# Kernel optimization log

Measured on AMD Instinct MI355X. Metric: run time of the kernel, lower is better.

Reference implementation:

```python
import jax, jax.numpy as jnp
import numpy as np
from jax import lax

SCALE = 1.0
DENSE = 4
ITERS = 5


def setup_inputs() -> dict:
    key = jax.random.key(0)
    k1, k2, k3 = jax.random.split(key, 3)
    N, C, H, W = 32, 3, 512, 512
    A = 512
    data = jax.random.normal(k1, (N, C, H, W), dtype=jnp.float32)
    attx = jax.random.uniform(k2, (N, A), dtype=jnp.float32)
    atty = jax.random.uniform(k3, (N, A), dtype=jnp.float32)
    return {"data": data, "attx": attx, "atty": atty}


def _water_fill(attx, atty, out_size, out_sizey, in_size):
    # iterative water-filling clamp: 5 sequential max/min/sum/update passes
    att_size = attx.shape[1]
    att_sizey = atty.shape[1]
    thr0 = (SCALE * DENSE * in_size) / att_size
    ax = attx * out_size
    ay = atty * out_sizey
    for j in range(ITERS):
        mx = jnp.max(ax, axis=1, keepdims=True)
        my = jnp.max(ay, axis=1, keepdims=True)
        thr = jnp.minimum(mx, my)
        if j == 0:
            thr = jnp.minimum(thr, thr0)
        ax = jnp.minimum(ax, thr)
        ay = jnp.minimum(ay, thr)
        ax = ax + (out_size - jnp.sum(ax, axis=1, keepdims=True)) / att_size
        ay = ay + (out_sizey - jnp.sum(ay, axis=1, keepdims=True)) / att_sizey
    # as in the source: first element forced to 1 before cumsum
    ax = ax.at[:, 0].set(1.0)
    ay = ay.at[:, 0].set(1.0)
    return jnp.cumsum(ax, axis=1), jnp.cumsum(ay, axis=1), ax, ay


def _coords(att, cs, out_n):
    # inverse-CDF mapping: for each of out_n uniform steps of the sampled axis,
    # find the source bin in cumsum cs and interpolate -> coord in [-1,1]
    A = att.shape[1]
    step = cs[:, -1] / out_n                                   # (N,)
    t = jnp.arange(1, out_n + 1, dtype=cs.dtype)[None, :] * step[:, None]  # (N,out_n)

    def per_sample(cs_n, att_n, t_n):
        j = jnp.clip(jnp.searchsorted(cs_n, t_n, side='left'), 0, A - 1)
        prev = jnp.where(j > 0, cs_n[jnp.maximum(j - 1, 0)], 0.0)
        frac = (t_n - prev) / jnp.maximum(att_n[j], 1e-12)
        return (j.astype(cs_n.dtype) + frac) / A * 2.0 - 1.0

    return jax.vmap(per_sample)(cs, att, t)


def _grid_sample(data, grid):
    # F.grid_sample, bilinear, padding_mode='zeros', align_corners=False
    N, C, H, W = data.shape
    x = (grid[..., 0] + 1.0) * (W / 2.0) - 0.5   # (N,Ho,Wo)
    y = (grid[..., 1] + 1.0) * (H / 2.0) - 0.5
    x0 = jnp.floor(x)
    y0 = jnp.floor(y)
    x1 = x0 + 1.0
    y1 = y0 + 1.0
    wx1 = x - x0
    wx0 = 1.0 - wx1
    wy1 = y - y0
    wy0 = 1.0 - wy1

    def gather(ix, iy):
        valid = (ix >= 0) & (ix < W) & (iy >= 0) & (iy < H)
        ixc = jnp.clip(ix, 0, W - 1).astype(jnp.int32)
        iyc = jnp.clip(iy, 0, H - 1).astype(jnp.int32)
        v = jax.vmap(lambda d, iy_n, ix_n: d[:, iy_n, ix_n])(data, iyc, ixc)  # (N,C,Ho,Wo)
        return v * valid[:, None, :, :].astype(data.dtype)

    out = (gather(x0, y0) * (wx0 * wy0)[:, None]
           + gather(x1, y0) * (wx1 * wy0)[:, None]
           + gather(x0, y1) * (wx0 * wy1)[:, None]
           + gather(x1, y1) * (wx1 * wy1)[:, None])
    return out


def reference(data, attx, atty):
    N, C, H, W = data.shape
    out_size = int(H * SCALE)
    out_sizey = int(W * SCALE)
    # grid is built from detached attention (data.detach()/att.detach() in source)
    ax_ = lax.stop_gradient(attx)
    ay_ = lax.stop_gradient(atty)
    csx, csy, ax, ay = _water_fill(ax_, ay_, out_size, out_sizey, H)
    gy = _coords(ax, csx, out_size)    # height coords, (N,out_size)
    gx = _coords(ay, csy, out_sizey)   # width coords,  (N,out_sizey)
    grid = jnp.stack([
        jnp.broadcast_to(gx[:, None, :], (N, out_size, out_sizey)),
        jnp.broadcast_to(gy[:, :, None], (N, out_size, out_sizey)),
    ], axis=-1)  # (N,Ho,Wo,2)
    grid = lax.stop_gradient(grid)
    sampled = _grid_sample(data, grid)
    return sampled, grid
```

## Files before the change

kernel.cpp:

```cpp
#include <hip/hip_runtime.h>
#include <hip/hip_bf16.h>

#define AN 512
#define NB 32
#define HW 512

__device__ __forceinline__ float waveMax(float v) {
    #pragma unroll
    for (int off = 32; off > 0; off >>= 1) v = fmaxf(v, __shfl_xor(v, off, 64));
    return v;
}
__device__ __forceinline__ float waveSum(float v) {
    #pragma unroll
    for (int off = 32; off > 0; off >>= 1) v += __shfl_xor(v, off, 64);
    return v;
}

__global__ __launch_bounds__(512) void waterfill_coords_kernel(
    const float* __restrict__ attx, const float* __restrict__ atty,
    float* __restrict__ gx, float* __restrict__ gy)
{
    __shared__ float axs[AN], ays[AN], csx[AN], csy[AN];
    __shared__ float wrx[8], wry[8];
    const int n = blockIdx.x;
    const int t = threadIdx.x;
    const int wid = t >> 6;

    float ax = attx[n * AN + t] * 512.0f;
    float ay = atty[n * AN + t] * 512.0f;

    for (int j = 0; j < 5; ++j) {
        float mx = waveMax(ax), my = waveMax(ay);
        if ((t & 63) == 0) { wrx[wid] = mx; wry[wid] = my; }
        __syncthreads();
        float Mx = wrx[0], My = wry[0];
        #pragma unroll
        for (int i = 1; i < 8; ++i) { Mx = fmaxf(Mx, wrx[i]); My = fmaxf(My, wry[i]); }
        float thr = fminf(Mx, My);
        if (j == 0) thr = fminf(thr, 4.0f);
        ax = fminf(ax, thr);
        ay = fminf(ay, thr);

        float sx = waveSum(ax), sy = waveSum(ay);
        __syncthreads();
        if ((t & 63) == 0) { wrx[wid] = sx; wry[wid] = sy; }
        __syncthreads();
        float Sx = 0.0f, Sy = 0.0f;
        #pragma unroll
        for (int i = 0; i < 8; ++i) { Sx += wrx[i]; Sy += wry[i]; }
        ax += (512.0f - Sx) / 512.0f;
        ay += (512.0f - Sy) / 512.0f;
        __syncthreads();
    }

    if (t == 0) { ax = 1.0f; ay = 1.0f; }
    axs[t] = ax; ays[t] = ay; csx[t] = ax; csy[t] = ay;
    __syncthreads();

    #pragma unroll
    for (int s = 1; s < AN; s <<= 1) {
        float vx = (t >= s) ? csx[t - s] : 0.0f;
        float vy = (t >= s) ? csy[t - s] : 0.0f;
        __syncthreads();
        csx[t] += vx; csy[t] += vy;
        __syncthreads();
    }

    {
        float step = csx[AN - 1] / 512.0f;
        float tv = (float)(t + 1) * step;
        int lo = 0, hi = AN;
        while (lo < hi) { int mid = (lo + hi) >> 1; if (csx[mid] < tv) lo = mid + 1; else hi = mid; }
        int j = lo > (AN - 1) ? (AN - 1) : lo;
        float prev = (j > 0) ? csx[j - 1] : 0.0f;
        float frac = (tv - prev) / fmaxf(axs[j], 1e-12f);
        gy[n * AN + t] = ((float)j + frac) * (2.0f / 512.0f) - 1.0f;
    }
    {
        float step = csy[AN - 1] / 512.0f;
        float tv = (float)(t + 1) * step;
        int lo = 0, hi = AN;
        while (lo < hi) { int mid = (lo + hi) >> 1; if (csy[mid] < tv) lo = mid + 1; else hi = mid; }
        int j = lo > (AN - 1) ? (AN - 1) : lo;
        float prev = (j > 0) ? csy[j - 1] : 0.0f;
        float frac = (tv - prev) / fmaxf(ays[j], 1e-12f);
        gx[n * AN + t] = ((float)j + frac) * (2.0f / 512.0f) - 1.0f;
    }
}

__global__ __launch_bounds__(256) void grid_sample_kernel(
    const float* __restrict__ data, const float* __restrict__ gx,
    const float* __restrict__ gy, float* __restrict__ outS,
    float* __restrict__ outG)
{
    __shared__ float rows[6][HW];
    const int t  = threadIdx.x;
    const int ho = blockIdx.x;
    const int n  = blockIdx.y;

    const float gyv = gy[n * AN + ho];
    const float y   = (gyv + 1.0f) * 256.0f - 0.5f;
    const float y0f = floorf(y);
    const float wy1 = y - y0f, wy0 = 1.0f - wy1;
    const float vy0 = ((y0f >= 0.0f) & (y0f < 512.0f)) ? 1.0f : 0.0f;
    const float vy1 = ((y0f >= -1.0f) & (y0f < 511.0f)) ? 1.0f : 0.0f;
    const int y0 = (int)fminf(fmaxf(y0f, 0.0f), 511.0f);
    const int y1 = (int)fminf(fmaxf(y0f + 1.0f, 0.0f), 511.0f);

    const float* base = data + (size_t)n * 3 * HW * HW;
    #pragma unroll
    for (int r = 0; r < 3; ++r) {
        const int idx = r * 256 + t;
        const int row = idx >> 7;
        const int col = idx & 127;
        const int yy  = (row < 3) ? y0 : y1;
        const int c   = (row < 3) ? row : row - 3;
        float4 v = ((const float4*)(base + ((size_t)c * HW + yy) * HW))[col];
        ((float4*)&rows[row][0])[col] = v;
    }
    __syncthreads();

    const float2 gx2 = ((const float2*)(gx + n * AN))[t];
    const float xg[2] = {gx2.x, gx2.y};
    float res[3][2];

    #pragma unroll
    for (int k = 0; k < 2; ++k) {
        const float gxv = xg[k];
        const float x   = (gxv + 1.0f) * 256.0f - 0.5f;
        const float x0f = floorf(x);
        const float wx1 = x - x0f, wx0 = 1.0f - wx1;
        const float vx0 = ((x0f >= 0.0f) & (x0f < 512.0f)) ? 1.0f : 0.0f;
        const float vx1 = ((x0f >= -1.0f) & (x0f < 511.0f)) ? 1.0f : 0.0f;
        const int x0 = (int)fminf(fmaxf(x0f, 0.0f), 511.0f);
        const int x1 = (int)fminf(fmaxf(x0f + 1.0f, 0.0f), 511.0f);
        const float w00 = wx0 * wy0 * vx0 * vy0;
        const float w10 = wx1 * wy0 * vx1 * vy0;
        const float w01 = wx0 * wy1 * vx0 * vy1;
        const float w11 = wx1 * wy1 * vx1 * vy1;
        #pragma unroll
        for (int c = 0; c < 3; ++c) {
            res[c][k] = rows[c][x0] * w00 + rows[c][x1] * w10
                      + rows[3 + c][x0] * w01 + rows[3 + c][x1] * w11;
        }
    }

    const int wo = 2 * t;
    const size_t o = (((size_t)n * 3) * HW + ho) * HW + wo;
    #pragma unroll
    for (int c = 0; c < 3; ++c)
        *(float2*)(outS + o + (size_t)c * HW * HW) = make_float2(res[c][0], res[c][1]);

    *(float4*)(outG + (((size_t)n * HW + ho) * HW + wo) * 2) =
        make_float4(gx2.x, gyv, gx2.y, gyv);
}

extern "C" void kernel_launch(void* const* d_in, const int* in_sizes, int n_in,
                              void* d_out, int out_size, void* d_ws, size_t ws_size,
                              hipStream_t stream) {
    const float* data = (const float*)d_in[0];
    const float* attx = (const float*)d_in[1];
    const float* atty = (const float*)d_in[2];

    float* gx = (float*)d_ws;
    float* gy = gx + NB * AN;

    float* outS = (float*)d_out;
    float* outG = outS + (size_t)NB * 3 * HW * HW;

    waterfill_coords_kernel<<<NB, AN, 0, stream>>>(attx, atty, gx, gy);

    dim3 grid(HW, NB);
    grid_sample_kernel<<<grid, 256, 0, stream>>>(data, gx, gy, outS, outG);
}
```

Baseline: 246.7 us.

## Use direct global-to-LDS loads, XCD-aware block remap, and wave-shuffle prefix scan

The grid-sample kernel now fills its shared row buffer with the global_load_lds builtin, copying straight from global memory into LDS without passing through registers. It also linearizes the grid and remaps block IDs so that consecutive blocks on each XCD cover contiguous rows and images. The waterfill kernel drops redundant barriers by using separate max and sum scratch arrays, replaces the block-wide Hillis-Steele scan with a wave-shuffle scan plus per-wave offsets, and runs the two binary searches interleaved with a fixed trip count. These changes aim to cut register staging, L2 locality misses and synchronization, but depend on 16-byte global_load_lds support and on correct wave-uniform LDS addressing.

```diff
diff --git a/kernel.cpp b/kernel.cpp
--- a/kernel.cpp
+++ b/kernel.cpp
@@ -21,69 +21,85 @@
     float* __restrict__ gx, float* __restrict__ gy)
 {
     __shared__ float axs[AN], ays[AN], csx[AN], csy[AN];
-    __shared__ float wrx[8], wry[8];
+    __shared__ float wmx[8], wmy[8], wsx[8], wsy[8], wtx[8], wty[8];
     const int n = blockIdx.x;
     const int t = threadIdx.x;
     const int wid = t >> 6;
+    const int lane = t & 63;
 
     float ax = attx[n * AN + t] * 512.0f;
     float ay = atty[n * AN + t] * 512.0f;
 
+    #pragma unroll
     for (int j = 0; j < 5; ++j) {
         float mx = waveMax(ax), my = waveMax(ay);
-        if ((t & 63) == 0) { wrx[wid] = mx; wry[wid] = my; }
+        if (lane == 0) { wmx[wid] = mx; wmy[wid] = my; }
         __syncthreads();
-        float Mx = wrx[0], My = wry[0];
+        float Mx = wmx[0], My = wmy[0];
         #pragma unroll
-        for (int i = 1; i < 8; ++i) { Mx = fmaxf(Mx, wrx[i]); My = fmaxf(My, wry[i]); }
+        for (int i = 1; i < 8; ++i) { Mx = fmaxf(Mx, wmx[i]); My = fmaxf(My, wmy[i]); }
         float thr = fminf(Mx, My);
         if (j == 0) thr = fminf(thr, 4.0f);
         ax = fminf(ax, thr);
         ay = fminf(ay, thr);
 
         float sx = waveSum(ax), sy = waveSum(ay);
-        __syncthreads();
-        if ((t & 63) == 0) { wrx[wid] = sx; wry[wid] = sy; }
+        if (lane == 0) { wsx[wid] = sx; wsy[wid] = sy; }
         __syncthreads();
         float Sx = 0.0f, Sy = 0.0f;
         #pragma unroll
-        for (int i = 0; i < 8; ++i) { Sx += wrx[i]; Sy += wry[i]; }
-        ax += (512.0f - Sx) / 512.0f;
-        ay += (512.0f - Sy) / 512.0f;
-        __syncthreads();
+        for (int i = 0; i < 8; ++i) { Sx += wsx[i]; Sy += wsy[i]; }
+        ax += (512.0f - Sx) * (1.0f / 512.0f);
+        ay += (512.0f - Sy) * (1.0f / 512.0f);
     }
 
     if (t == 0) { ax = 1.0f; ay = 1.0f; }
-    axs[t] = ax; ays[t] = ay; csx[t] = ax; csy[t] = ay;
+    axs[t] = ax; ays[t] = ay;
+
+    float cx = ax, cy = ay;
+    #pragma unroll
+    for (int off = 1; off < 64; off <<= 1) {
+        float ux = __shfl_up(cx, off, 64);
+        float uy = __shfl_up(cy, off, 64);
+        if (lane >= off) { cx += ux; cy += uy; }
+    }
+    if (lane == 63) { wtx[wid] = cx; wty[wid] = cy; }
+    __syncthreads();
+    float px = 0.0f, py = 0.0f;
+    #pragma unroll
+    for (int i = 0; i < 8; ++i) {
+        if (i < wid) { px += wtx[i]; py += wty[i]; }
+    }
+    cx += px; cy += py;
+    csx[t] = cx; csy[t] = cy;
     __syncthreads();
 
+    const float stepx = csx[AN - 1] * (1.0f / 512.0f);
+    const float stepy = csy[AN - 1] * (1.0f / 512.0f);
+    const float tvx = (float)(t + 1) * stepx;
+    const float tvy = (float)(t + 1) * stepy;
+    int lox = 0, hix = AN, loy = 0, hiy = AN;
     #pragma unroll
-    for (int s = 1; s < AN; s <<= 1) {
-        float vx = (t >= s) ? csx[t - s] : 0.0f;
-        float vy = (t >= s) ? csy[t - s] : 0.0f;
-        __syncthreads();
-        csx[t] += vx; csy[t] += vy;
-        __syncthreads();
+    for (int s = 0; s < 9; ++s) {
+        const int mx_ = (lox + hix) >> 1;
+        const int my_ = (loy + hiy) >> 1;
+        const float vx = csx[mx_];
+        const float vy = csy[my_];
+        if (vx < tvx) lox = mx_ + 1; else hix = mx_;
+        if (vy < tvy) loy = my_ + 1; else hiy = my_;
     }
-
+    if (lox < hix && csx[lox] < tvx) ++lox;
+    if (loy < hiy && csy[loy] < tvy) ++loy;
     {
-        float step = csx[AN - 1] / 512.0f;
-        float tv = (float)(t + 1) * step;
-        int lo = 0, hi = AN;
-        while (lo < hi) { int mid = (lo + hi) >> 1; if (csx[mid] < tv) lo = mid + 1; else hi = mid; }
-        int j = lo > (AN - 1) ? (AN - 1) : lo;
-        float prev = (j > 0) ? csx[j - 1] : 0.0f;
-        float frac = (tv - prev) / fmaxf(axs[j], 1e-12f);
+        const int j = lox > (AN - 1) ? (AN - 1) : lox;
+        const float prev = (j > 0) ? csx[j - 1] : 0.0f;
+        const float frac = (tvx - prev) / fmaxf(axs[j], 1e-12f);
         gy[n * AN + t] = ((float)j + frac) * (2.0f / 512.0f) - 1.0f;
     }
     {
-        float step = csy[AN - 1] / 512.0f;
-        float tv = (float)(t + 1) * step;
-        int lo = 0, hi = AN;
-        while (lo < hi) { int mid = (lo + hi) >> 1; if (csy[mid] < tv) lo = mid + 1; else hi = mid; }
-        int j = lo > (AN - 1) ? (AN - 1) : lo;
-        float prev = (j > 0) ? csy[j - 1] : 0.0f;
-        float frac = (tv - prev) / fmaxf(ays[j], 1e-12f);
+        const int j = loy > (AN - 1) ? (AN - 1) : loy;
+        const float prev = (j > 0) ? csy[j - 1] : 0.0f;
+        const float frac = (tvy - prev) / fmaxf(ays[j], 1e-12f);
         gx[n * AN + t] = ((float)j + frac) * (2.0f / 512.0f) - 1.0f;
     }
 }
@@ -93,10 +109,14 @@
     const float* __restrict__ gy, float* __restrict__ outS,
     float* __restrict__ outG)
 {
-    __shared__ float rows[6][HW];
-    const int t  = threadIdx.x;
-    const int ho = blockIdx.x;
-    const int n  = blockIdx.y;
+    __shared__ __align__(16) float rows[6][HW];
+    const int t   = threadIdx.x;
+    const int lid = blockIdx.x;
+    const int wg  = (lid & 7) * 2048 + (lid >> 3);
+    const int n   = wg >> 9;
+    const int ho  = wg & 511;
+    const int wid = t >> 6;
+    const int lane = t & 63;
 
     const float gyv = gy[n * AN + ho];
     const float y   = (gyv + 1.0f) * 256.0f - 0.5f;
@@ -110,13 +130,16 @@
     const float* base = data + (size_t)n * 3 * HW * HW;
     #pragma unroll
     for (int r = 0; r < 3; ++r) {
-        const int idx = r * 256 + t;
-        const int row = idx >> 7;
-        const int col = idx & 127;
-        const int yy  = (row < 3) ? y0 : y1;
-        const int c   = (row < 3) ? row : row - 3;
-        float4 v = ((const float4*)(base + ((size_t)c * HW + yy) * HW))[col];
-        ((float4*)&rows[row][0])[col] = v;
+        const int idx0 = r * 256 + (wid << 6);
+        const int row0 = idx0 >> 7;
+        const int col0 = idx0 & 127;
+        const int yy   = (row0 < 3) ? y0 : y1;
+        const int c    = (row0 < 3) ? row0 : row0 - 3;
+        const float* g = base + ((size_t)c * HW + yy) * HW + ((col0 + lane) << 2);
+        __builtin_amdgcn_global_load_lds(
+            (const __attribute__((address_space(1))) void*)g,
+            (__attribute__((address_space(3))) void*)(&rows[row0][col0 << 2]),
+            16, 0, 0);
     }
     __syncthreads();
 
@@ -170,6 +193,5 @@
 
     waterfill_coords_kernel<<<NB, AN, 0, stream>>>(attx, atty, gx, gy);
 
-    dim3 grid(HW, NB);
-    grid_sample_kernel<<<grid, 256, 0, stream>>>(data, gx, gy, outS, outG);
+    grid_sample_kernel<<<NB * HW, 256, 0, stream>>>(data, gx, gy, outS, outG);
 }
```

Measured after the change: 250.1 us. Within noise of the previous version (+1.4%).
